# Performance work log

Measured on AMD Instinct MI355X. Metric: run time of the kernel, lower is better.

## Reference

```python
import jax, jax.numpy as jnp
import numpy as np

H = 2048
W = 2048

# 2x2 derivative kernels (classic Lucas-Kanade / Horn-Schunck estimates)
_KX = np.array([[-1.0, 1.0], [-1.0, 1.0]], dtype=np.float32) * 0.25
_KY = np.array([[-1.0, -1.0], [1.0, 1.0]], dtype=np.float32) * 0.25
_KT = np.array([[1.0, 1.0], [1.0, 1.0]], dtype=np.float32) * 0.25


def _conv2d(x, k, padding):
    # x: (H, W), k: (kh, kw) -> (H', W')
    return jax.lax.conv_general_dilated(
        x[None, None], k[None, None].astype(x.dtype), (1, 1), padding
    )[0, 0]


def _deriv(img, k):
    # replicate-pad bottom/right so the 2x2 valid conv returns (H, W)
    p = jnp.pad(img, ((0, 1), (0, 1)), mode='edge')
    return _conv2d(p, jnp.asarray(k), 'VALID')


def setup_inputs() -> dict:
    key = jax.random.key(0)
    k1, k2 = jax.random.split(key)
    image_prev = jax.random.uniform(k1, (1, 1, H, W), dtype=jnp.float32)
    image_next = jax.random.uniform(k2, (1, 1, H, W), dtype=jnp.float32)
    return {"image_prev": image_prev, "image_next": image_next, "window_size": 15}


def reference(image_prev, image_next, window_size):
    prev = image_prev[0, 0]  # (H, W); original code only uses batch 0, channel 0
    nxt = image_next[0, 0]

    fx = 0.5 * (_deriv(prev, _KX) + _deriv(nxt, _KX))
    fy = 0.5 * (_deriv(prev, _KY) + _deriv(nxt, _KY))
    ft = _deriv(nxt, _KT) - _deriv(prev, _KT)

    w = int(window_size)
    ones = jnp.ones((w, w), dtype=fx.dtype)

    def box(f):
        # window sum with zero padding == ZeroPad2d(n) + w x w sliding sum
        return _conv2d(f, ones, 'SAME')

    Axx = box(fx * fx)
    Axy = box(fx * fy)
    Ayy = box(fy * fy)
    bx = box(fx * ft)
    by = box(fy * ft)

    det = Axx * Ayy - Axy * Axy
    valid = det != 0
    safe_det = jnp.where(valid, det, jnp.ones_like(det))
    # [[Axx,Axy],[Axy,Ayy]]^{-1} @ [bx, by]
    u = jnp.where(valid, (Ayy * bx - Axy * by) / safe_det, 0.0)
    v = jnp.where(valid, (Axx * by - Axy * bx) / safe_det, 0.0)

    return jnp.stack([u, v])[None]  # (1, 2, H, W)
```

## Files before the change

kernel.cpp:

```cpp
#include <hip/hip_runtime.h>


constexpr int IH  = 2048;
constexpr int IW  = 2048;
constexpr int RAD = 7;
constexpr int WIN = 15;
constexpr int NT  = 256;
constexpr int RB  = 4;
constexpr int BR  = 4 * RB;
constexpr int SROWS = BR + WIN;
constexpr int SW  = 112;
constexpr int SCAN = RB + WIN - 1;
constexpr int NSTRIP = 19;
constexpr int NGRP  = IH / BR;
constexpr int NXCD  = 8;
constexpr int CHUNK = NGRP / NXCD;

__device__ __forceinline__ int clampi(int v, int lo, int hi) {
    return v < lo ? lo : (v > hi ? hi : v);
}

struct Row { float sp0, sp1, dt0, dt1; };

template<bool SUB, bool XE>
__device__ __forceinline__ void accum(float V[5][2], const Row& A, const Row& B,
                                      int t, bool ok, bool rep2) {
    const float g0 = A.sp0 + B.sp0, g1 = A.sp1 + B.sp1;
    const float m0 = B.sp0 - A.sp0, m1 = B.sp1 - A.sp1;
    const float e0 = A.dt0 + B.dt0, e1 = A.dt1 + B.dt1;
    float g2 = __shfl(g0, t + 1);
    float m2 = __shfl(m0, t + 1);
    float e2 = __shfl(e0, t + 1);
    if constexpr (XE) {
        g2 = rep2 ? g1 : g2; m2 = rep2 ? m1 : m2; e2 = rep2 ? e1 : e2;
    }
    float fx0 = g1 - g0, fy0 = m0 + m1, ft0 = e0 + e1;
    float fx1 = g2 - g1, fy1 = m1 + m2, ft1 = e1 + e2;
    if constexpr (XE) {
        fx0 = ok ? fx0 : 0.f; fy0 = ok ? fy0 : 0.f; ft0 = ok ? ft0 : 0.f;
        fx1 = ok ? fx1 : 0.f; fy1 = ok ? fy1 : 0.f; ft1 = ok ? ft1 : 0.f;
    }
    if constexpr (!SUB) {
        V[0][0] += fx0 * fx0; V[1][0] += fx0 * fy0; V[2][0] += fy0 * fy0;
        V[3][0] += fx0 * ft0; V[4][0] += fy0 * ft0;
        V[0][1] += fx1 * fx1; V[1][1] += fx1 * fy1; V[2][1] += fy1 * fy1;
        V[3][1] += fx1 * ft1; V[4][1] += fy1 * ft1;
    } else {
        V[0][0] -= fx0 * fx0; V[1][0] -= fx0 * fy0; V[2][0] -= fy0 * fy0;
        V[3][0] -= fx0 * ft0; V[4][0] -= fy0 * ft0;
        V[0][1] -= fx1 * fx1; V[1][1] -= fx1 * fy1; V[2][1] -= fy1 * fy1;
        V[3][1] -= fx1 * ft1; V[4][1] -= fy1 * ft1;
    }
}

template<bool XE>
__device__ __forceinline__ void scan_body(const float2* __restrict__ sp,
                                          const float2* __restrict__ dt,
                                          float* __restrict__ out,
                                          int c0, int R, int wid, int t) {
    const int r0  = R + wid * RB;
    const int kb  = wid * RB;
    const int pcb = c0 - 8 + 2 * t;
    bool ok = true, rep2 = false;
    if constexpr (XE) {
        ok   = ((unsigned)pcb < (unsigned)IW);
        rep2 = (pcb + 2 >= IW) && ok;
    }

    auto ldrow = [&](int k) -> Row {
        const float2 a = sp[k * 64 + t];
        const float2 b = dt[k * 64 + t];
        Row r; r.sp0 = a.x; r.sp1 = a.y; r.dt0 = b.x; r.dt1 = b.y; return r;
    };

    float V[5][2] = {};
    Row A = ldrow(kb), B = ldrow(kb + 1), C = ldrow(kb + 2);

    #pragma unroll
    for (int sr = 0; sr < SCAN; ++sr) {
        const int pr = r0 - RAD + sr;

        Row nC;
        const bool doE = (sr <= 15);
        if (doE) nC = ldrow(kb + sr + 3);
        Row XA, XB;
        const bool doX = (sr >= WIN);
        if (doX) { XA = ldrow(kb + sr - 15); XB = ldrow(kb + sr - 14); }

        if (pr >= 0 && pr < IH)
            accum<false, XE>(V, A, B, t, ok, rep2);
        if (doX && (pr - WIN) >= 0)
            accum<true, XE>(V, XA, XB, t, ok, rep2);

        if (sr >= WIN - 1) {
            float a0[5], a1[5];
            #pragma unroll
            for (int p = 0; p < 5; ++p) {
                const float Pg = V[p][0] + V[p][1];
                float S = Pg + __shfl(Pg, t + 1);
                S += __shfl(S, t + 2);
                S += __shfl(S, t + 4);
                const float q0 = __shfl(V[p][0], t + 8);
                a0[p] = S - V[p][0];
                a1[p] = (S - Pg) + q0;
            }
            const float det0 = a0[0] * a0[2] - a0[1] * a0[1];
            const float rd0  = __builtin_amdgcn_rcpf(det0) * 2.0f;
            const bool  k0   = (det0 != 0.f);
            const float det1 = a1[0] * a1[2] - a1[1] * a1[1];
            const float rd1  = __builtin_amdgcn_rcpf(det1) * 2.0f;
            const bool  k1   = (det1 != 0.f);
            float2 qu, qv;
            qu.x = k0 ? (a0[2] * a0[3] - a0[1] * a0[4]) * rd0 : 0.f;
            qv.x = k0 ? (a0[0] * a0[4] - a0[1] * a0[3]) * rd0 : 0.f;
            qu.y = k1 ? (a1[2] * a1[3] - a1[1] * a1[4]) * rd1 : 0.f;
            qv.y = k1 ? (a1[0] * a1[4] - a1[1] * a1[3]) * rd1 : 0.f;

            const int i  = r0 + sr - (WIN - 1);
            const int x0 = c0 + 2 * t;
            if ((2 * t < SW) && (x0 < IW)) {
                *reinterpret_cast<float2*>(out + (size_t)i * IW + x0) = qu;
                *reinterpret_cast<float2*>(out + (size_t)IH * IW + (size_t)i * IW + x0) = qv;
            }
        }

        A = B; B = C; if (doE) C = nC;
    }
}

__global__ __launch_bounds__(NT)
void lk_kernel(const float* __restrict__ Pimg, const float* __restrict__ Nimg,
               float* __restrict__ out) {
    __shared__ float4 s_sp[SROWS][32];
    __shared__ float4 s_dt[SROWS][32];

    const int bid   = blockIdx.x;
    const int xcd   = bid & 7;
    const int idx   = bid >> 3;
    const int strip = idx / CHUNK;
    const int pos   = idx % CHUNK;
    const int bg    = xcd * CHUNK + pos;
    const int c0    = strip * SW;
    const int R     = bg * BR;

    const int jq = threadIdx.x & 31;
    const int rr = threadIdx.x >> 5;
    const int gc = c0 - 8 + 4 * jq;
    const bool in4 = (gc >= 0) && (gc + 3 < IW);
    #pragma unroll
    for (int k0 = 0; k0 < SROWS; k0 += 8) {
        const int k = k0 + rr;
        if (k < SROWS) {
            const int row = clampi(R - RAD + k, 0, IH - 1);
            const float* rp = Pimg + (size_t)row * IW;
            const float* rn = Nimg + (size_t)row * IW;
            float4 p, n;
            if (in4) {
                p = *reinterpret_cast<const float4*>(rp + gc);
                n = *reinterpret_cast<const float4*>(rn + gc);
            } else {
                const int g0 = clampi(gc,     0, IW - 1);
                const int g1 = clampi(gc + 1, 0, IW - 1);
                const int g2 = clampi(gc + 2, 0, IW - 1);
                const int g3 = clampi(gc + 3, 0, IW - 1);
                p = make_float4(rp[g0], rp[g1], rp[g2], rp[g3]);
                n = make_float4(rn[g0], rn[g1], rn[g2], rn[g3]);
            }
            s_sp[k][jq] = make_float4(p.x + n.x, p.y + n.y, p.z + n.z, p.w + n.w);
            s_dt[k][jq] = make_float4(n.x - p.x, n.y - p.y, n.z - p.z, n.w - p.w);
        }
    }
    __syncthreads();

    const int wid = threadIdx.x >> 6;
    const int t   = threadIdx.x & 63;
    const float2* sp = reinterpret_cast<const float2*>(&s_sp[0][0]);
    const float2* dt = reinterpret_cast<const float2*>(&s_dt[0][0]);
    if (strip == 0 || strip == NSTRIP - 1)
        scan_body<true >(sp, dt, out, c0, R, wid, t);
    else
        scan_body<false>(sp, dt, out, c0, R, wid, t);
}

extern "C" void kernel_launch(void* const* d_in, const int* in_sizes, int n_in,
                              void* d_out, int out_size, void* d_ws, size_t ws_size,
                              hipStream_t stream) {
    (void)in_sizes; (void)n_in; (void)d_ws; (void)ws_size; (void)out_size;
    const float* prev = (const float*)d_in[0];
    const float* nxt  = (const float*)d_in[1];
    float* out        = (float*)d_out;
    dim3 grid(NSTRIP * NGRP);
    dim3 block(NT);
    hipLaunchKernelGGL(lk_kernel, grid, block, 0, stream, prev, nxt, out);
}
```

Baseline: 33.67 us.

## Use taller 32-row bands with 512 threads and specialize vertical-edge bounds checks

Each block now covers 32 output rows with 8 wavefronts instead of 16 rows with 4, so the shared-memory halo (15 extra rows) is amortized over more output rows. This cuts redundant global loads and input preprocessing. A second template flag removes the per-row vertical bounds checks for interior bands. In exchange, blocks are larger and use more shared memory, there are half as many blocks, and the number of kernel instantiations grows to four.

```diff
diff --git a/kernel.cpp b/kernel.cpp
--- a/kernel.cpp
+++ b/kernel.cpp
@@ -5,16 +5,16 @@
 constexpr int IW  = 2048;
 constexpr int RAD = 7;
 constexpr int WIN = 15;
-constexpr int NT  = 256;
-constexpr int RB  = 4;
-constexpr int BR  = 4 * RB;
-constexpr int SROWS = BR + WIN;
+constexpr int NT  = 512;
 constexpr int SW  = 112;
-constexpr int SCAN = RB + WIN - 1;
+constexpr int RBW = 4;
+constexpr int TH  = 32;
+constexpr int SROWS = TH + WIN + 1;
+constexpr int SCAN  = RBW + WIN - 1;
 constexpr int NSTRIP = 19;
-constexpr int NGRP  = IH / BR;
-constexpr int NXCD  = 8;
-constexpr int CHUNK = NGRP / NXCD;
+constexpr int NBANDS = IH / TH;
+constexpr int NXCD   = 8;
+constexpr int CHUNK  = NBANDS / NXCD;
 
 __device__ __forceinline__ int clampi(int v, int lo, int hi) {
     return v < lo ? lo : (v > hi ? hi : v);
@@ -53,13 +53,11 @@
     }
 }
 
-template<bool XE>
+template<bool XE, bool YE>
 __device__ __forceinline__ void scan_body(const float2* __restrict__ sp,
                                           const float2* __restrict__ dt,
                                           float* __restrict__ out,
-                                          int c0, int R, int wid, int t) {
-    const int r0  = R + wid * RB;
-    const int kb  = wid * RB;
+                                          int c0, int r0, int kb, int t) {
     const int pcb = c0 - 8 + 2 * t;
     bool ok = true, rep2 = false;
     if constexpr (XE) {
@@ -74,23 +72,29 @@
     };
 
     float V[5][2] = {};
-    Row A = ldrow(kb), B = ldrow(kb + 1), C = ldrow(kb + 2);
+    Row E0 = ldrow(kb), E1 = ldrow(kb + 1), E2 = ldrow(kb + 2);
 
     #pragma unroll
     for (int sr = 0; sr < SCAN; ++sr) {
         const int pr = r0 - RAD + sr;
 
-        Row nC;
+        Row nE;
         const bool doE = (sr <= 15);
-        if (doE) nC = ldrow(kb + sr + 3);
-        Row XA, XB;
-        const bool doX = (sr >= WIN);
-        if (doX) { XA = ldrow(kb + sr - 15); XB = ldrow(kb + sr - 14); }
-
-        if (pr >= 0 && pr < IH)
-            accum<false, XE>(V, A, B, t, ok, rep2);
-        if (doX && (pr - WIN) >= 0)
-            accum<true, XE>(V, XA, XB, t, ok, rep2);
+        if (doE) nE = ldrow(kb + sr + 3);
+
+        bool enter_ok = true;
+        if constexpr (YE) enter_ok = (pr >= 0) && (pr < IH);
+        if (enter_ok) accum<false, XE>(V, E0, E1, t, ok, rep2);
+
+        if (sr >= WIN) {
+            bool exit_ok = true;
+            if constexpr (YE) exit_ok = (pr - WIN) >= 0;
+            if (exit_ok) {
+                const Row XA = ldrow(kb + sr - 15);
+                const Row XB = ldrow(kb + sr - 14);
+                accum<true, XE>(V, XA, XB, t, ok, rep2);
+            }
+        }
 
         if (sr >= WIN - 1) {
             float a0[5], a1[5];
@@ -124,7 +128,7 @@
             }
         }
 
-        A = B; B = C; if (doE) C = nC;
+        E0 = E1; E1 = E2; if (doE) E2 = nE;
     }
 }
 
@@ -139,18 +143,18 @@
     const int idx   = bid >> 3;
     const int strip = idx / CHUNK;
     const int pos   = idx % CHUNK;
-    const int bg    = xcd * CHUNK + pos;
+    const int band  = xcd * CHUNK + pos;
     const int c0    = strip * SW;
-    const int R     = bg * BR;
-
-    const int jq = threadIdx.x & 31;
-    const int rr = threadIdx.x >> 5;
-    const int gc = c0 - 8 + 4 * jq;
-    const bool in4 = (gc >= 0) && (gc + 3 < IW);
-    #pragma unroll
-    for (int k0 = 0; k0 < SROWS; k0 += 8) {
-        const int k = k0 + rr;
-        if (k < SROWS) {
+    const int R     = band * TH;
+
+    {
+        const int jq = threadIdx.x & 31;
+        const int rr = threadIdx.x >> 5;
+        const int gc = c0 - 8 + 4 * jq;
+        const bool in4 = (gc >= 0) && (gc + 3 < IW);
+        #pragma unroll
+        for (int k0 = 0; k0 < SROWS; k0 += 16) {
+            const int k   = k0 + rr;
             const int row = clampi(R - RAD + k, 0, IH - 1);
             const float* rp = Pimg + (size_t)row * IW;
             const float* rn = Nimg + (size_t)row * IW;
@@ -174,12 +178,16 @@
 
     const int wid = threadIdx.x >> 6;
     const int t   = threadIdx.x & 63;
+    const int r0  = R + RBW * wid;
+    const int kb  = RBW * wid;
     const float2* sp = reinterpret_cast<const float2*>(&s_sp[0][0]);
     const float2* dt = reinterpret_cast<const float2*>(&s_dt[0][0]);
-    if (strip == 0 || strip == NSTRIP - 1)
-        scan_body<true >(sp, dt, out, c0, R, wid, t);
-    else
-        scan_body<false>(sp, dt, out, c0, R, wid, t);
+    const bool xe = (strip == 0) || (strip == NSTRIP - 1);
+    const bool ye = (band == 0) || (band == NBANDS - 1);
+    if (!xe && !ye)      scan_body<false, false>(sp, dt, out, c0, r0, kb, t);
+    else if (xe && !ye)  scan_body<true,  false>(sp, dt, out, c0, r0, kb, t);
+    else if (!xe)        scan_body<false, true >(sp, dt, out, c0, r0, kb, t);
+    else                 scan_body<true,  true >(sp, dt, out, c0, r0, kb, t);
 }
 
 extern "C" void kernel_launch(void* const* d_in, const int* in_sizes, int n_in,
@@ -189,7 +197,7 @@
     const float* prev = (const float*)d_in[0];
     const float* nxt  = (const float*)d_in[1];
     float* out        = (float*)d_out;
-    dim3 grid(NSTRIP * NGRP);
+    dim3 grid(NSTRIP * NBANDS);
     dim3 block(NT);
     hipLaunchKernelGGL(lk_kernel, grid, block, 0, stream, prev, nxt, out);
 }
```

New measurement: 33.09 us. About the same (-1.7%).
